# Optimization experiments

Hardware: AMD Instinct MI355X
Metric: run time of the kernel (lower is better)

Reference implementation:

```python
import jax, jax.numpy as jnp
import numpy as np

B, N, D, H, HD, C = 2, 2048, 2048, 16, 128, 128  # batch, seq, embed, heads, head_dim, chunk
EPS = 1e-6


def setup_inputs() -> dict:
    key = jax.random.key(0)
    ks = jax.random.split(key, 9)
    s = 0.02
    x = jax.random.normal(ks[0], (B, N, D), jnp.float32)
    # per-head negative log decay (lambda = exp(log_decay) in (0,1))
    log_decay = -jax.random.uniform(ks[1], (H,), jnp.float32, minval=0.01, maxval=1.0)
    Wq = jax.random.normal(ks[2], (D, D), jnp.float32) * s
    Wk = jax.random.normal(ks[3], (D, D), jnp.float32) * s
    Wv = jax.random.normal(ks[4], (D, D), jnp.float32) * s
    Wo = jax.random.normal(ks[5], (D, D), jnp.float32) * s
    Wg1 = jax.random.normal(ks[6], (D, HD), jnp.float32) * s
    Wg2 = jax.random.normal(ks[7], (HD, D), jnp.float32) * s
    norm_w = jnp.ones((D,), jnp.float32)
    return dict(x=x, log_decay=log_decay, Wq=Wq, Wk=Wk, Wv=Wv, Wo=Wo,
                Wg1=Wg1, Wg2=Wg2, norm_w=norm_w)


def _lasd(q, k, v, ld):
    # causal linear attention with per-head scalar log-decay, chunked scan.
    # q,k,v: [B,N,H,HD]; ld: [H] (negative). Recurrence: S_t = exp(ld)*S_{t-1} + k_t v_t^T; o_t = q_t @ S_t
    nc = N // C
    to_chunks = lambda t: t.reshape(B, nc, C, H, HD).transpose(1, 0, 3, 2, 4)  # [nc,B,H,C,HD]
    qc, kc, vc = map(to_chunks, (q, k, v))
    i = jnp.arange(C, dtype=jnp.float32)
    diff = i[:, None] - i[None, :]                     # [C,C]
    Dm = jnp.exp(jnp.where(diff >= 0, ld[:, None, None] * diff, -jnp.inf))  # [H,C,C]
    dq = jnp.exp(ld[:, None] * (i + 1.0))              # [H,C] decay applied to q vs chunk-start state
    dk = jnp.exp(ld[:, None] * (C - 1.0 - i))          # [H,C] decay applied to k for state update
    dS = jnp.exp(ld * C)                               # [H]   chunk-level state decay

    def step(S, qkv):
        qb, kb, vb = qkv                               # [B,H,C,HD]
        attn = jnp.einsum('bhid,bhjd->bhij', qb, kb) * Dm
        o = jnp.einsum('bhij,bhje->bhie', attn, vb)
        o = o + jnp.einsum('bhid,bhde->bhie', qb * dq[None, :, :, None], S)
        S = S * dS[None, :, None, None] + jnp.einsum('bhjd,bhje->bhde', kb * dk[None, :, :, None], vb)
        return S, o

    S0 = jnp.zeros((B, H, HD, HD), jnp.float32)
    _, o = jax.lax.scan(step, S0, (qc, kc, vc))        # [nc,B,H,C,HD]
    return o.transpose(1, 0, 3, 2, 4).reshape(B, N, H, HD)


def reference(x, log_decay, Wq, Wk, Wv, Wo, Wg1, Wg2, norm_w):
    silu = jax.nn.silu
    q = silu(x @ Wq).reshape(B, N, H, HD)
    k = silu(x @ Wk).reshape(B, N, H, HD)
    v = silu(x @ Wv).reshape(B, N, H, HD)
    o = _lasd(q, k, v, log_decay).reshape(B, N, D)
    gate = jax.nn.sigmoid((x @ Wg1) @ Wg2)             # two stacked linears, no nonlinearity between
    o = o * gate
    o = o * jax.lax.rsqrt(jnp.mean(o * o, axis=-1, keepdims=True) + EPS) * norm_w  # rmsnorm
    return o @ Wo
```

## Files before the change

### kernel.cpp

```cpp
#include <hip/hip_runtime.h>
#include <hip/hip_bf16.h>
#include <cstdint>
#include <cstddef>

#define B_   2
#define N_   2048
#define D_   2048
#define H_   16
#define HD_  128
#define C_   128
#define NC_  16
#define M_   4096
#define QKVG_ 8192

typedef __attribute__((ext_vector_type(8))) short bf16x8;
typedef __attribute__((ext_vector_type(4))) float f32x4;
typedef __attribute__((ext_vector_type(16))) float f32x16;

__device__ __forceinline__ uint16_t f2bf(float f){
  __hip_bfloat16 h = __float2bfloat16(f);
  return *reinterpret_cast<uint16_t*>(&h);
}
__device__ __forceinline__ float bf2f(uint16_t u){
  union { uint32_t i; float f; } v; v.i = ((uint32_t)u) << 16; return v.f;
}

__device__ __forceinline__ void async16(const uint16_t* g, uint16_t* l){
  __builtin_amdgcn_global_load_lds(
      (const __attribute__((address_space(1))) void*)g,
      (__attribute__((address_space(3))) void*)l, 16, 0, 0);
}

__device__ __forceinline__ int swz(int row, int c){
  return row*128 + ((((c >> 3) ^ row) & 15) << 3) + (c & 7);
}

__global__ __launch_bounds__(256)
void prep_weights(const float* __restrict__ Wq, const float* __restrict__ Wk,
                  const float* __restrict__ Wv, const float* __restrict__ Wo,
                  const float* __restrict__ Wg2, const float* __restrict__ Wg1,
                  uint16_t* __restrict__ WT, uint16_t* __restrict__ WoT,
                  uint16_t* __restrict__ Wg2T, uint16_t* __restrict__ Wg1b,
                  const float* __restrict__ x, uint16_t* __restrict__ xb)
{
  const int z = blockIdx.z;
  const int tx = threadIdx.x & 31;
  const int ty = threadIdx.x >> 5;
  __shared__ uint16_t tile[32][33];

  if (z == 6){
    const int r0 = blockIdx.y*64, c0 = blockIdx.x*32;
    const int cx = (threadIdx.x & 7)*4, ry = threadIdx.x >> 3;
    #pragma unroll
    for (int rr = 0; rr < 2; ++rr){
      int r = r0 + ry + rr*32;
      float4 f = *(const float4*)(x + (size_t)r*D_ + c0 + cx);
      ushort4 u;
      u.x = f2bf(f.x); u.y = f2bf(f.y); u.z = f2bf(f.z); u.w = f2bf(f.w);
      *(ushort4*)(xb + (size_t)r*D_ + c0 + cx) = u;
    }
    return;
  }

  if (z == 5){
    if (blockIdx.x >= 4) return;
    const int r0 = blockIdx.y*32, c0 = blockIdx.x*32;
    #pragma unroll
    for (int rr = 0; rr < 4; ++rr){
      int r = r0 + ty + rr*8;
      Wg1b[(size_t)r*HD_ + c0 + tx] = f2bf(Wg1[(size_t)r*HD_ + c0 + tx]);
    }
    return;
  }

  const float* src; uint16_t* dst; int R, Cc;
  if (z < 3)      { src = (z==0)?Wq:(z==1)?Wk:Wv; dst = WT + (size_t)z*D_*D_; R = D_; Cc = D_; }
  else if (z == 3){ src = Wo;  dst = WoT;  R = D_;  Cc = D_; }
  else            { if (blockIdx.y >= 4) return;
                    src = Wg2; dst = Wg2T; R = HD_; Cc = D_; }

  const int r0 = blockIdx.y*32, c0 = blockIdx.x*32;
  #pragma unroll
  for (int rr = 0; rr < 4; ++rr){
    int r = ty + rr*8;
    tile[r][tx] = f2bf(src[(size_t)(r0 + r)*Cc + c0 + tx]);
  }
  __syncthreads();
  #pragma unroll
  for (int rr = 0; rr < 4; ++rr){
    int r = ty + rr*8;
    dst[(size_t)(c0 + r)*R + r0 + tx] = tile[tx][r];
  }
}

template<int ACT, int OUTBF>
__global__ __launch_bounds__(256)
void gemm_bt2(const uint16_t* __restrict__ A, const uint16_t* __restrict__ Bt,
              void* __restrict__ Cout, int M, int Ncols, int K, int klen)
{
  __shared__ __align__(16) uint16_t As[128*64];
  __shared__ __align__(16) uint16_t Bs[128*64];
  const int t    = threadIdx.x;
  const int lane = t & 63, wave = t >> 6;
  const int wm = wave >> 1, wn = wave & 1;
  const int row0 = wm*64, col0 = wn*64;
  const int lm = lane & 31, lh = lane >> 5;

  const uint16_t* Ap = A  + (size_t)(blockIdx.y*128)*K;
  const uint16_t* Bp = Bt + (size_t)(blockIdx.x*128)*K;
  const int kbeg = blockIdx.z * klen;

  f32x16 acc[2][2];
  #pragma unroll
  for (int i = 0; i < 2; ++i)
    #pragma unroll
    for (int j = 0; j < 2; ++j)
      #pragma unroll
      for (int r = 0; r < 16; ++r) acc[i][j][r] = 0.f;

  const int srow = t >> 3;
  const int gch  = (t & 7) ^ (srow & 7);
  const size_t aoff0 = (size_t)srow*K + gch*8;

  for (int k0 = kbeg; k0 < kbeg + klen; k0 += 64){
    #pragma unroll
    for (int c = 0; c < 4; ++c){
      async16(Ap + (size_t)(c*32)*K + aoff0 + k0, As + c*2048 + t*8);
      async16(Bp + (size_t)(c*32)*K + aoff0 + k0, Bs + c*2048 + t*8);
    }
    __syncthreads();
    #pragma unroll
    for (int kh = 0; kh < 4; ++kh){
      bf16x8 af[2], bfr[2];
      const int ch = kh*2 + lh;
      #pragma unroll
      for (int i = 0; i < 2; ++i){
        int r = row0 + i*32 + lm;
        af[i] = *(const bf16x8*)(As + r*64 + ((ch ^ (r & 7)) << 3));
      }
      #pragma unroll
      for (int j = 0; j < 2; ++j){
        int r = col0 + j*32 + lm;
        bfr[j] = *(const bf16x8*)(Bs + r*64 + ((ch ^ (r & 7)) << 3));
      }
      #pragma unroll
      for (int i = 0; i < 2; ++i)
        #pragma unroll
        for (int j = 0; j < 2; ++j)
          acc[i][j] = __builtin_amdgcn_mfma_f32_32x32x16_bf16(af[i], bfr[j], acc[i][j], 0, 0, 0);
    }
    __syncthreads();
  }

  const int mode = (ACT == 3) ? ((blockIdx.x < 48) ? 1 : 2) : ACT;
  uint16_t* outb = (uint16_t*)Cout;
  float*    outf = (float*)Cout + (OUTBF ? 0 : (size_t)blockIdx.z*M*Ncols);
  #pragma unroll
  for (int i = 0; i < 2; ++i){
    #pragma unroll
    for (int j = 0; j < 2; ++j){
      #pragma unroll
      for (int r = 0; r < 16; ++r){
        int row = blockIdx.y*128 + row0 + i*32 + (r & 3) + 8*(r >> 2) + 4*lh;
        int col = blockIdx.x*128 + col0 + j*32 + lm;
        float v = acc[i][j][r];
        if (mode == 1)      v = v / (1.f + __expf(-v));
        else if (mode == 2) v = 1.f / (1.f + __expf(-v));
        size_t off = (size_t)row*Ncols + col;
        if (OUTBF) outb[off] = f2bf(v);
        else       outf[off] = v;
      }
    }
  }
}

template<int ACT, int OUTBF>
__global__ __launch_bounds__(512, 2)
void gemm256(const uint16_t* __restrict__ A, const uint16_t* __restrict__ Bt,
             void* __restrict__ Cout, int M, int Ncols, int K, int klen)
{
  __shared__ __align__(16) uint16_t As[4*256*32];
  __shared__ __align__(16) uint16_t Bs[4*256*32];
  const int t    = threadIdx.x;
  const int lane = t & 63, wave = t >> 6;
  const int wm = wave >> 2, wn = wave & 3;
  const int lm = lane & 31, lh = lane >> 5;
  const int sel = (lm >> 1) & 3;

  int arow[4], brow[2], sl[2];
  #pragma unroll
  for (int m = 0; m < 4; ++m) arow[m] = (wm*128 + m*32 + lm)*32;
  #pragma unroll
  for (int n = 0; n < 2; ++n) brow[n] = (wn*64 + n*32 + lm)*32;
  #pragma unroll
  for (int kk = 0; kk < 2; ++kk) sl[kk] = ((kk*2 + lh) ^ sel) << 3;

  const uint16_t* Ap = A  + (size_t)(blockIdx.y*256)*K;
  const uint16_t* Bp = Bt + (size_t)(blockIdx.x*256)*K;
  const int kbeg = blockIdx.z*klen;
  const int NTK  = klen >> 5;

  const int gch  = (t & 3) ^ ((t >> 3) & 3);
  const size_t srcoff = (size_t)(t >> 2)*K + gch*8;
  const int ldst = t*8;

  f32x16 acc[4][2];
  #pragma unroll
  for (int m = 0; m < 4; ++m)
    #pragma unroll
    for (int n = 0; n < 2; ++n)
      #pragma unroll
      for (int r = 0; r < 16; ++r) acc[m][n][r] = 0.f;

  auto stageA = [&](int j){
    const size_t ko = (size_t)kbeg + (size_t)j*32;
    uint16_t* d = As + (j & 3)*8192 + ldst;
    async16(Ap + srcoff + ko, d);
    async16(Ap + (size_t)128*K + srcoff + ko, d + 4096);
  };
  auto stageB = [&](int j){
    const size_t ko = (size_t)kbeg + (size_t)j*32;
    uint16_t* d = Bs + (j & 3)*8192 + ldst;
    async16(Bp + srcoff + ko, d);
    async16(Bp + (size_t)128*K + srcoff + ko, d + 4096);
  };

  stageA(0); stageB(0);
  stageA(1); stageB(1);
  stageA(2); stageB(2);
  asm volatile("s_waitcnt vmcnt(4)" ::: "memory");
  __builtin_amdgcn_s_barrier();
  asm volatile("" ::: "memory");

  bf16x8 af0[4], bf0[2], af1[4], bf1[2];
  #pragma unroll
  for (int m = 0; m < 4; ++m) af0[m] = *(const bf16x8*)(As + arow[m] + sl[0]);
  #pragma unroll
  for (int n = 0; n < 2; ++n) bf0[n] = *(const bf16x8*)(Bs + brow[n] + sl[0]);

  for (int kt = 0; kt < NTK; ++kt){
    const uint16_t* Ac = As + (kt & 3)*8192;
    const uint16_t* Bc = Bs + (kt & 3)*8192;
    const uint16_t* An = As + ((kt + 1) & 3)*8192;
    const uint16_t* Bn = Bs + ((kt + 1) & 3)*8192;

    #pragma unroll
    for (int m = 0; m < 4; ++m) af1[m] = *(const bf16x8*)(Ac + arow[m] + sl[1]);
    #pragma unroll
    for (int n = 0; n < 2; ++n) bf1[n] = *(const bf16x8*)(Bc + brow[n] + sl[1]);
    if (kt + 3 < NTK) stageA(kt + 3);
    asm volatile("s_waitcnt lgkmcnt(6)" ::: "memory");
    __builtin_amdgcn_sched_barrier(0);
    __builtin_amdgcn_s_setprio(1);
    #pragma unroll
    for (int m = 0; m < 4; ++m)
      #pragma unroll
      for (int n = 0; n < 2; ++n)
        acc[m][n] = __builtin_amdgcn_mfma_f32_32x32x16_bf16(af0[m], bf0[n], acc[m][n], 0, 0, 0);
    __builtin_amdgcn_s_setprio(0);

    if (kt + 1 < NTK){
      #pragma unroll
      for (int m = 0; m < 4; ++m) af0[m] = *(const bf16x8*)(An + arow[m] + sl[0]);
      #pragma unroll
      for (int n = 0; n < 2; ++n) bf0[n] = *(const bf16x8*)(Bn + brow[n] + sl[0]);
    }
    if (kt + 3 < NTK) stageB(kt + 3);
    if (kt + 1 < NTK) asm volatile("s_waitcnt lgkmcnt(6)" ::: "memory");
    else              asm volatile("s_waitcnt lgkmcnt(0)" ::: "memory");
    __builtin_amdgcn_sched_barrier(0);
    __builtin_amdgcn_s_setprio(1);
    #pragma unroll
    for (int m = 0; m < 4; ++m)
      #pragma unroll
      for (int n = 0; n < 2; ++n)
        acc[m][n] = __builtin_amdgcn_mfma_f32_32x32x16_bf16(af1[m], bf1[n], acc[m][n], 0, 0, 0);
    __builtin_amdgcn_s_setprio(0);

    if (kt + 3 < NTK)       asm volatile("s_waitcnt vmcnt(4)" ::: "memory");
    else if (kt + 3 == NTK) asm volatile("s_waitcnt vmcnt(0)" ::: "memory");
    __builtin_amdgcn_s_barrier();
    asm volatile("" ::: "memory");
  }

  const int mode = (ACT == 3) ? (((blockIdx.x << 8) < Ncols - 2048) ? 1 : 2) : ACT;
  uint16_t* outb = (uint16_t*)Cout;
  float*    outf = (float*)Cout + (OUTBF ? 0 : (size_t)blockIdx.z*M*Ncols);
  #pragma unroll
  for (int m = 0; m < 4; ++m){
    #pragma unroll
    for (int n = 0; n < 2; ++n){
      #pragma unroll
      for (int r = 0; r < 16; ++r){
        int row = blockIdx.y*256 + wm*128 + m*32 + (r & 3) + 8*(r >> 2) + 4*lh;
        int col = blockIdx.x*256 + wn*64  + n*32 + lm;
        float v = acc[m][n][r];
        if (mode == 1)      v = v / (1.f + __expf(-v));
        else if (mode == 2) v = 1.f / (1.f + __expf(-v));
        size_t off = (size_t)row*Ncols + col;
        if (OUTBF) outb[off] = f2bf(v);
        else       outf[off] = v;
      }
    }
  }
}

__global__ __launch_bounds__(256)
void chunk_state_kernel(const uint16_t* __restrict__ qkvg,
                        const float* __restrict__ log_decay, uint16_t* __restrict__ MsumT)
{
  __shared__ __align__(16) uint16_t vT[128*128];
  __shared__ __align__(16) uint16_t kT[128*128];
  const int h = blockIdx.x, b = blockIdx.y, ic = blockIdx.z;
  const int t    = threadIdx.x;
  const int lane = t & 63, wave = t >> 6;
  const int wm = wave >> 1, wn = wave & 1;
  const int e0 = wm*64, d0 = wn*64;
  const int lr = lane & 15, kq = lane >> 4;
  const float ld = log_decay[h];
  const size_t rowbase = (size_t)b*N_ + (size_t)ic*C_;
  const uint16_t* kb = qkvg + (size_t)D_;
  const uint16_t* vb = qkvg + (size_t)2*D_;

  #pragma unroll 4
  for (int it = 0; it < 64; ++it){
    int idx = t + it*256;
    int j = idx >> 7, e = idx & 127;
    uint16_t vv = vb[(rowbase + j)*QKVG_ + h*HD_ + e];
    float kf = bf2f(kb[(rowbase + j)*QKVG_ + h*HD_ + e]) * __expf(ld * (float)(C_ - 1 - j));
    vT[swz(e, j)] = vv;
    kT[swz(e, j)] = f2bf(kf);
  }
  __syncthreads();

  const f32x4 zero = {0.f, 0.f, 0.f, 0.f};
  f32x4 acc[4][4];
  #pragma unroll
  for (int i = 0; i < 4; ++i)
    #pragma unroll
    for (int j = 0; j < 4; ++j) acc[i][j] = zero;

  #pragma unroll
  for (int kt = 0; kt < 4; ++kt){
    bf16x8 af[4], bfr[4];
    #pragma unroll
    for (int i = 0; i < 4; ++i)
      af[i]  = *(const bf16x8*)(vT + swz(e0 + i*16 + lr, kt*32 + kq*8));
    #pragma unroll
    for (int j = 0; j < 4; ++j)
      bfr[j] = *(const bf16x8*)(kT + swz(d0 + j*16 + lr, kt*32 + kq*8));
    #pragma unroll
    for (int i = 0; i < 4; ++i)
      #pragma unroll
      for (int j = 0; j < 4; ++j)
        acc[i][j] = __builtin_amdgcn_mfma_f32_16x16x32_bf16(af[i], bfr[j], acc[i][j], 0, 0, 0);
  }

  uint16_t* Mout = MsumT + (((size_t)ic*B_ + b)*H_ + h)*(size_t)(HD_*HD_);
  #pragma unroll
  for (int i = 0; i < 4; ++i)
    #pragma unroll
    for (int j = 0; j < 4; ++j)
      #pragma unroll
      for (int r = 0; r < 4; ++r)
        Mout[(size_t)(e0 + i*16 + kq*4 + r)*HD_ + d0 + j*16 + lr] = f2bf(acc[i][j][r]);
}

__global__ __launch_bounds__(256)
void scan_kernel(const uint16_t* __restrict__ MsumT, const float* __restrict__ log_decay,
                 uint16_t* __restrict__ StT)
{
  const int h = blockIdx.x, b = blockIdx.y;
  const float ld = log_decay[h];
  const float dS = __expf(ld * (float)C_);
  const int base_e = blockIdx.z*2048;
  float cur[8];
  #pragma unroll
  for (int r = 0; r < 8; ++r) cur[r] = 0.f;
  for (int i = 0; i < NC_; ++i){
    const size_t base = (((size_t)i*B_ + b)*H_ + h)*(size_t)(HD_*HD_) + base_e;
    #pragma unroll
    for (int r = 0; r < 8; ++r){
      int idx = threadIdx.x + r*256;
      StT[base + idx] = f2bf(cur[r]);
      cur[r] = cur[r]*dS + bf2f(MsumT[base + idx]);
    }
  }
}

__global__ __launch_bounds__(256)
void attn_kernel(const uint16_t* __restrict__ qkvg, const uint16_t* __restrict__ StT,
                 const float* __restrict__ log_decay, float* __restrict__ o_attn)
{
  __shared__ __align__(16) uint16_t Ps[128*128];
  __shared__ __align__(16) uint16_t vT[128*128];
  const int h = blockIdx.x, b = blockIdx.y, ic = blockIdx.z;
  const int t    = threadIdx.x;
  const int lane = t & 63, wave = t >> 6;
  const int wm = wave >> 1, wn = wave & 1;
  const int row0 = wm*64, col0 = wn*64;
  const int lr = lane & 15, kq = lane >> 4;
  const float ld = log_decay[h];
  const size_t rowbase = (size_t)b*N_ + (size_t)ic*C_;
  const uint16_t* qb = qkvg;
  const uint16_t* kb = qkvg + (size_t)D_;
  const uint16_t* vb = qkvg + (size_t)2*D_;

  #pragma unroll 4
  for (int it = 0; it < 64; ++it){
    int idx = t + it*256;
    int j = idx >> 7, e = idx & 127;
    vT[swz(e, j)] = vb[(rowbase + j)*QKVG_ + h*HD_ + e];
  }

  const f32x4 zero = {0.f, 0.f, 0.f, 0.f};
  f32x4 acc[4][4];
  #pragma unroll
  for (int i = 0; i < 4; ++i)
    #pragma unroll
    for (int j = 0; j < 4; ++j) acc[i][j] = zero;

  #pragma unroll
  for (int kt = 0; kt < 4; ++kt){
    bf16x8 af[4], bfr[4];
    #pragma unroll
    for (int i = 0; i < 4; ++i)
      af[i]  = *(const bf16x8*)(qb + (rowbase + row0 + i*16 + lr)*QKVG_ + h*HD_ + kt*32 + kq*8);
    #pragma unroll
    for (int j = 0; j < 4; ++j)
      bfr[j] = *(const bf16x8*)(kb + (rowbase + col0 + j*16 + lr)*QKVG_ + h*HD_ + kt*32 + kq*8);
    #pragma unroll
    for (int i = 0; i < 4; ++i)
      #pragma unroll
      for (int j = 0; j < 4; ++j)
        acc[i][j] = __builtin_amdgcn_mfma_f32_16x16x32_bf16(af[i], bfr[j], acc[i][j], 0, 0, 0);
  }
  #pragma unroll
  for (int i = 0; i < 4; ++i)
    #pragma unroll
    for (int j = 0; j < 4; ++j)
      #pragma unroll
      for (int r = 0; r < 4; ++r){
        int row = row0 + i*16 + kq*4 + r;
        int col = col0 + j*16 + lr;
        int dlt = row - col;
        float f = (dlt >= 0) ? __expf(ld * (float)dlt) : 0.f;
        Ps[swz(row, col)] = f2bf(acc[i][j][r] * f);
      }

  #pragma unroll
  for (int i = 0; i < 4; ++i)
    #pragma unroll
    for (int j = 0; j < 4; ++j) acc[i][j] = zero;
  const uint16_t* Sb = StT + (((size_t)ic*B_ + b)*H_ + h)*(size_t)(HD_*HD_);
  #pragma unroll
  for (int kt = 0; kt < 4; ++kt){
    bf16x8 af[4], bfr[4];
    #pragma unroll
    for (int i = 0; i < 4; ++i)
      af[i]  = *(const bf16x8*)(qb + (rowbase + row0 + i*16 + lr)*QKVG_ + h*HD_ + kt*32 + kq*8);
    #pragma unroll
    for (int j = 0; j < 4; ++j)
      bfr[j] = *(const bf16x8*)(Sb + (size_t)(col0 + j*16 + lr)*HD_ + kt*32 + kq*8);
    #pragma unroll
    for (int i = 0; i < 4; ++i)
      #pragma unroll
      for (int j = 0; j < 4; ++j)
        acc[i][j] = __builtin_amdgcn_mfma_f32_16x16x32_bf16(af[i], bfr[j], acc[i][j], 0, 0, 0);
  }
  #pragma unroll
  for (int i = 0; i < 4; ++i)
    #pragma unroll
    for (int r = 0; r < 4; ++r){
      float dqv = __expf(ld * (float)(row0 + i*16 + kq*4 + r + 1));
      #pragma unroll
      for (int j = 0; j < 4; ++j) acc[i][j][r] *= dqv;
    }

  __syncthreads();

  #pragma unroll
  for (int kt = 0; kt < 4; ++kt){
    bf16x8 af[4], bfr[4];
    #pragma unroll
    for (int i = 0; i < 4; ++i)
      af[i]  = *(const bf16x8*)(Ps + swz(row0 + i*16 + lr, kt*32 + kq*8));
    #pragma unroll
    for (int j = 0; j < 4; ++j)
      bfr[j] = *(const bf16x8*)(vT + swz(col0 + j*16 + lr, kt*32 + kq*8));
    #pragma unroll
    for (int i = 0; i < 4; ++i)
      #pragma unroll
      for (int j = 0; j < 4; ++j)
        acc[i][j] = __builtin_amdgcn_mfma_f32_16x16x32_bf16(af[i], bfr[j], acc[i][j], 0, 0, 0);
  }

  #pragma unroll
  for (int i = 0; i < 4; ++i)
    #pragma unroll
    for (int j = 0; j < 4; ++j)
      #pragma unroll
      for (int r = 0; r < 4; ++r){
        int row = row0 + i*16 + kq*4 + r;
        int col = col0 + j*16 + lr;
        o_attn[(rowbase + row)*D_ + h*HD_ + col] = acc[i][j][r];
      }
}

__global__ __launch_bounds__(256)
void gate_norm_kernel(const float* __restrict__ o_attn, const uint16_t* __restrict__ qkvg,
                      const float* __restrict__ norm_w, uint16_t* __restrict__ on)
{
  const int row = blockIdx.x;
  const int t = threadIdx.x;
  const int c1 = t*4, c2 = 1024 + t*4;
  const float*    orow = o_attn + (size_t)row*D_;
  const uint16_t* grow = qkvg + (size_t)row*QKVG_ + 3*D_;
  float4  o1 = *(const float4*)(orow + c1);
  float4  o2 = *(const float4*)(orow + c2);
  ushort4 g1 = *(const ushort4*)(grow + c1);
  ushort4 g2 = *(const ushort4*)(grow + c2);
  float v[8];
  v[0] = o1.x*bf2f(g1.x); v[1] = o1.y*bf2f(g1.y); v[2] = o1.z*bf2f(g1.z); v[3] = o1.w*bf2f(g1.w);
  v[4] = o2.x*bf2f(g2.x); v[5] = o2.y*bf2f(g2.y); v[6] = o2.z*bf2f(g2.z); v[7] = o2.w*bf2f(g2.w);
  float s = 0.f;
  #pragma unroll
  for (int k = 0; k < 8; ++k) s += v[k]*v[k];
  #pragma unroll
  for (int off = 32; off > 0; off >>= 1) s += __shfl_down(s, off);
  __shared__ float red[4];
  if ((t & 63) == 0) red[t >> 6] = s;
  __syncthreads();
  float total = red[0] + red[1] + red[2] + red[3];
  float scale = rsqrtf(total * (1.f/(float)D_) + 1e-6f);
  float4 w1 = *(const float4*)(norm_w + c1);
  float4 w2 = *(const float4*)(norm_w + c2);
  ushort4 b1, b2;
  b1.x = f2bf(v[0]*scale*w1.x); b1.y = f2bf(v[1]*scale*w1.y);
  b1.z = f2bf(v[2]*scale*w1.z); b1.w = f2bf(v[3]*scale*w1.w);
  b2.x = f2bf(v[4]*scale*w2.x); b2.y = f2bf(v[5]*scale*w2.y);
  b2.z = f2bf(v[6]*scale*w2.z); b2.w = f2bf(v[7]*scale*w2.w);
  *(ushort4*)(on + (size_t)row*D_ + c1) = b1;
  *(ushort4*)(on + (size_t)row*D_ + c2) = b2;
}

extern "C" void kernel_launch(void* const* d_in, const int* in_sizes, int n_in,
                              void* d_out, int out_size, void* d_ws, size_t ws_size,
                              hipStream_t stream) {
  const float* x         = (const float*)d_in[0];
  const float* log_decay = (const float*)d_in[1];
  const float* Wq        = (const float*)d_in[2];
  const float* Wk        = (const float*)d_in[3];
  const float* Wv        = (const float*)d_in[4];
  const float* Wo        = (const float*)d_in[5];
  const float* Wg1       = (const float*)d_in[6];
  const float* Wg2       = (const float*)d_in[7];
  const float* norm_w    = (const float*)d_in[8];
  float* out = (float*)d_out;

  uint8_t* p = (uint8_t*)d_ws;
  uint16_t* xb    = (uint16_t*)p; p += (size_t)M_*D_*2;
  uint16_t* WT    = (uint16_t*)p; p += (size_t)QKVG_*D_*2;
  uint16_t* WoT   = (uint16_t*)p; p += (size_t)D_*D_*2;
  uint16_t* Wg1b  = (uint16_t*)p; p += (size_t)D_*HD_*2;
  uint16_t* Wg2T  = (uint16_t*)p; p += (size_t)D_*HD_*2;
  uint16_t* qkvg  = (uint16_t*)p; p += (size_t)M_*QKVG_*2;
  uint16_t* MsumT = (uint16_t*)p; p += (size_t)NC_*B_*H_*HD_*HD_*2;
  uint16_t* StT   = (uint16_t*)p; p += (size_t)NC_*B_*H_*HD_*HD_*2;
  float*    o_att = (float*)WT;
  uint16_t* on    = xb;

  prep_weights<<<dim3(64, 64, 7), 256, 0, stream>>>(Wq, Wk, Wv, Wo, Wg2, Wg1,
                                                    WT, WoT, Wg2T, Wg1b, x, xb);

  gemm_bt2<0,1><<<dim3(D_/128, D_/128, 1), 256, 0, stream>>>(
      Wg2T, Wg1b, WT + (size_t)3*D_*D_, D_, D_, HD_, HD_);

  gemm256<3,1><<<dim3(QKVG_/256, M_/256, 1), 512, 0, stream>>>(
      xb, WT, qkvg, M_, QKVG_, D_, D_);

  chunk_state_kernel<<<dim3(H_, B_, NC_), 256, 0, stream>>>(qkvg, log_decay, MsumT);
  scan_kernel<<<dim3(H_, B_, 8), 256, 0, stream>>>(MsumT, log_decay, StT);
  attn_kernel<<<dim3(H_, B_, NC_), 256, 0, stream>>>(qkvg, StT, log_decay, o_att);

  gate_norm_kernel<<<M_, 256, 0, stream>>>(o_att, qkvg, norm_w, on);
  gemm_bt2<0,0><<<dim3(D_/128, M_/128, 1), 256, 0, stream>>>(
      on, WoT, out, M_, D_, D_, D_);
}
```

Measured before the change: 400.2 us.

## Vectorize chunk loads, reswizzle LDS transpose, and remap GEMM blocks across XCDs

Adds an XCD-aware block index remap to both GEMM kernels so neighbouring tiles land on the same XCD and share L2. The K/V transpose staging in the chunk-sum and attention kernels now loads 8 bf16 values per 16-byte access instead of one element at a time. The LDS swizzle gains an extra XOR term so the scattered transposed writes hit fewer bank conflicts. The scan kernel moves to vectorized 8-wide loads and stores with a contiguous per-thread layout. Risks are a remap that could hurt locality for some grid shapes, and scatter writes that may still conflict in LDS.

```diff
diff --git a/kernel.cpp b/kernel.cpp
--- a/kernel.cpp
+++ b/kernel.cpp
@@ -31,8 +31,18 @@
       (__attribute__((address_space(3))) void*)l, 16, 0, 0);
 }
 
-__device__ __forceinline__ int swz(int row, int c){
-  return row*128 + ((((c >> 3) ^ row) & 15) << 3) + (c & 7);
+__device__ __forceinline__ int swz(int e, int j){
+  return e*128 + ((((j >> 3) ^ e ^ (e >> 3)) & 15) << 3) + (j & 7);
+}
+
+__device__ __forceinline__ void xcd_swz(int& bx, int& by){
+  const int gx = gridDim.x, nwg = gx*gridDim.y;
+  int flat = by*gx + bx;
+  if ((nwg & 7) == 0){
+    const int cpx = nwg >> 3;
+    flat = (flat & 7)*cpx + (flat >> 3);
+  }
+  bx = flat % gx; by = flat / gx;
 }
 
 __global__ __launch_bounds__(256)
@@ -106,8 +116,11 @@
   const int row0 = wm*64, col0 = wn*64;
   const int lm = lane & 31, lh = lane >> 5;
 
-  const uint16_t* Ap = A  + (size_t)(blockIdx.y*128)*K;
-  const uint16_t* Bp = Bt + (size_t)(blockIdx.x*128)*K;
+  int bx = blockIdx.x, by = blockIdx.y;
+  xcd_swz(bx, by);
+
+  const uint16_t* Ap = A  + (size_t)(by*128)*K;
+  const uint16_t* Bp = Bt + (size_t)(bx*128)*K;
   const int kbeg = blockIdx.z * klen;
 
   f32x16 acc[2][2];
@@ -152,7 +165,7 @@
     __syncthreads();
   }
 
-  const int mode = (ACT == 3) ? ((blockIdx.x < 48) ? 1 : 2) : ACT;
+  const int mode = (ACT == 3) ? ((bx < 48) ? 1 : 2) : ACT;
   uint16_t* outb = (uint16_t*)Cout;
   float*    outf = (float*)Cout + (OUTBF ? 0 : (size_t)blockIdx.z*M*Ncols);
   #pragma unroll
@@ -161,8 +174,8 @@
     for (int j = 0; j < 2; ++j){
       #pragma unroll
       for (int r = 0; r < 16; ++r){
-        int row = blockIdx.y*128 + row0 + i*32 + (r & 3) + 8*(r >> 2) + 4*lh;
-        int col = blockIdx.x*128 + col0 + j*32 + lm;
+        int row = by*128 + row0 + i*32 + (r & 3) + 8*(r >> 2) + 4*lh;
+        int col = bx*128 + col0 + j*32 + lm;
         float v = acc[i][j][r];
         if (mode == 1)      v = v / (1.f + __expf(-v));
         else if (mode == 2) v = 1.f / (1.f + __expf(-v));
@@ -187,6 +200,9 @@
   const int lm = lane & 31, lh = lane >> 5;
   const int sel = (lm >> 1) & 3;
 
+  int bx = blockIdx.x, by = blockIdx.y;
+  xcd_swz(bx, by);
+
   int arow[4], brow[2], sl[2];
   #pragma unroll
   for (int m = 0; m < 4; ++m) arow[m] = (wm*128 + m*32 + lm)*32;
@@ -195,8 +211,8 @@
   #pragma unroll
   for (int kk = 0; kk < 2; ++kk) sl[kk] = ((kk*2 + lh) ^ sel) << 3;
 
-  const uint16_t* Ap = A  + (size_t)(blockIdx.y*256)*K;
-  const uint16_t* Bp = Bt + (size_t)(blockIdx.x*256)*K;
+  const uint16_t* Ap = A  + (size_t)(by*256)*K;
+  const uint16_t* Bp = Bt + (size_t)(bx*256)*K;
   const int kbeg = blockIdx.z*klen;
   const int NTK  = klen >> 5;
 
@@ -283,7 +299,7 @@
     asm volatile("" ::: "memory");
   }
 
-  const int mode = (ACT == 3) ? (((blockIdx.x << 8) < Ncols - 2048) ? 1 : 2) : ACT;
+  const int mode = (ACT == 3) ? (((bx << 8) < Ncols - 2048) ? 1 : 2) : ACT;
   uint16_t* outb = (uint16_t*)Cout;
   float*    outf = (float*)Cout + (OUTBF ? 0 : (size_t)blockIdx.z*M*Ncols);
   #pragma unroll
@@ -292,8 +308,8 @@
     for (int n = 0; n < 2; ++n){
       #pragma unroll
       for (int r = 0; r < 16; ++r){
-        int row = blockIdx.y*256 + wm*128 + m*32 + (r & 3) + 8*(r >> 2) + 4*lh;
-        int col = blockIdx.x*256 + wn*64  + n*32 + lm;
+        int row = by*256 + wm*128 + m*32 + (r & 3) + 8*(r >> 2) + 4*lh;
+        int col = bx*256 + wn*64  + n*32 + lm;
         float v = acc[m][n][r];
         if (mode == 1)      v = v / (1.f + __expf(-v));
         else if (mode == 2) v = 1.f / (1.f + __expf(-v));
@@ -322,14 +338,20 @@
   const uint16_t* kb = qkvg + (size_t)D_;
   const uint16_t* vb = qkvg + (size_t)2*D_;
 
-  #pragma unroll 4
-  for (int it = 0; it < 64; ++it){
+  #pragma unroll
+  for (int it = 0; it < 8; ++it){
     int idx = t + it*256;
-    int j = idx >> 7, e = idx & 127;
-    uint16_t vv = vb[(rowbase + j)*QKVG_ + h*HD_ + e];
-    float kf = bf2f(kb[(rowbase + j)*QKVG_ + h*HD_ + e]) * __expf(ld * (float)(C_ - 1 - j));
-    vT[swz(e, j)] = vv;
-    kT[swz(e, j)] = f2bf(kf);
+    int j = idx >> 4, ee = (idx & 15)*8;
+    const size_t g = (rowbase + j)*QKVG_ + h*HD_ + ee;
+    bf16x8 kv = *(const bf16x8*)(kb + g);
+    bf16x8 vv = *(const bf16x8*)(vb + g);
+    float dk = __expf(ld * (float)(C_ - 1 - j));
+    #pragma unroll
+    for (int u = 0; u < 8; ++u){
+      int s = swz(ee + u, j);
+      vT[s] = (uint16_t)(unsigned short)vv[u];
+      kT[s] = f2bf(bf2f((uint16_t)(unsigned short)kv[u]) * dk);
+    }
   }
   __syncthreads();
 
@@ -373,18 +395,20 @@
   const int h = blockIdx.x, b = blockIdx.y;
   const float ld = log_decay[h];
   const float dS = __expf(ld * (float)C_);
-  const int base_e = blockIdx.z*2048;
+  const size_t off = (size_t)blockIdx.z*2048 + (size_t)threadIdx.x*8;
   float cur[8];
   #pragma unroll
-  for (int r = 0; r < 8; ++r) cur[r] = 0.f;
+  for (int u = 0; u < 8; ++u) cur[u] = 0.f;
   for (int i = 0; i < NC_; ++i){
-    const size_t base = (((size_t)i*B_ + b)*H_ + h)*(size_t)(HD_*HD_) + base_e;
-    #pragma unroll
-    for (int r = 0; r < 8; ++r){
-      int idx = threadIdx.x + r*256;
-      StT[base + idx] = f2bf(cur[r]);
-      cur[r] = cur[r]*dS + bf2f(MsumT[base + idx]);
-    }
+    const size_t base = (((size_t)i*B_ + b)*H_ + h)*(size_t)(HD_*HD_) + off;
+    bf16x8 m = *(const bf16x8*)(MsumT + base);
+    bf16x8 s;
+    #pragma unroll
+    for (int u = 0; u < 8; ++u) s[u] = (short)f2bf(cur[u]);
+    *(bf16x8*)(StT + base) = s;
+    #pragma unroll
+    for (int u = 0; u < 8; ++u)
+      cur[u] = cur[u]*dS + bf2f((uint16_t)(unsigned short)m[u]);
   }
 }
 
@@ -406,11 +430,14 @@
   const uint16_t* kb = qkvg + (size_t)D_;
   const uint16_t* vb = qkvg + (size_t)2*D_;
 
-  #pragma unroll 4
-  for (int it = 0; it < 64; ++it){
+  #pragma unroll
+  for (int it = 0; it < 8; ++it){
     int idx = t + it*256;
-    int j = idx >> 7, e = idx & 127;
-    vT[swz(e, j)] = vb[(rowbase + j)*QKVG_ + h*HD_ + e];
+    int j = idx >> 4, ee = (idx & 15)*8;
+    bf16x8 vv = *(const bf16x8*)(vb + (rowbase + j)*QKVG_ + h*HD_ + ee);
+    #pragma unroll
+    for (int u = 0; u < 8; ++u)
+      vT[swz(ee + u, j)] = (uint16_t)(unsigned short)vv[u];
   }
 
   const f32x4 zero = {0.f, 0.f, 0.f, 0.f};
```

Result: slower. 412.6 us (+3.1%).
